# Optimization experiments

Hardware: AMD Instinct MI355X
Metric: run time of the kernel (lower is better)

Reference implementation:

```python
import jax, jax.numpy as jnp
import numpy as np
from jax.scipy.special import logsumexp

B, L, M, D = 8192, 1024, 128, 2  # batch, hilbert.size, bond dim, local_size
MACHINE_POW = 2


def setup_inputs() -> dict:
    key = jax.random.key(0)
    k1, k2 = jax.random.split(key)
    # configurations in the zero-magnetization sector: each row is a permutation
    # of L//2 zeros and L//2 ones (constrained HomogeneousHilbert)
    base = jnp.tile(jnp.arange(D, dtype=jnp.int32), L // D)  # (L,)
    inputs = jax.vmap(lambda k: jax.random.permutation(k, base))(jax.random.split(k1, B))
    # variational parameters epsilon: (local_size, M, size); centered at 1 so the
    # length-L multiplicative cache chain stays in fp32 range
    epsilon = 1.0 + 0.02 * jax.random.normal(k2, (D, M, L), dtype=jnp.float32)
    return {"inputs": inputs, "epsilon": epsilon}


def _conditionals(inputs, epsilon):
    # inputs: (B, L) int in [0, D); epsilon: (D, M, L)
    Bn, Ln = inputs.shape
    Dn, Mn, _ = epsilon.shape
    half = Ln // 2

    def scan_fun(carry, index):
        cache, n_spins = carry                       # (B, D, M), (B, D)
        prev = inputs[:, (index - 1) % Ln]           # (B,) previous-site state
        params_i = epsilon[:, :, index]              # (D, M)
        # irregular gather: cache[b, prev[b], :]
        gathered = jnp.take_along_axis(cache, prev[:, None, None], axis=1)[:, 0, :]  # (B, M)
        prods = params_i[None, :, :] * gathered[:, None, :]  # (B, D, M)
        log_psi = jnp.sum(prods, axis=-1)            # (B, D) sum over bond dim
        n_spins = jnp.where(index > 0,
                            n_spins + jax.nn.one_hot(prev, Dn, dtype=jnp.int32),
                            n_spins)
        # zero-magnetization renormalization: -inf once a local state is exhausted
        renorm = jnp.log(jnp.heaviside((half - n_spins).astype(log_psi.dtype), 0.0))
        return (prods, n_spins), log_psi + renorm

    cache0 = jnp.ones((Bn, Dn, Mn), epsilon.dtype)
    n0 = jnp.zeros((Bn, Dn), jnp.int32)
    _, log_psi = jax.lax.scan(scan_fun, (cache0, n0), jnp.arange(Ln))
    return jnp.transpose(log_psi, (1, 0, 2))  # (B, L, D)


def reference(inputs, epsilon):
    lp = _conditionals(inputs, epsilon)  # (B, L, D)
    # normalize conditionals over local states (machine_pow = 2)
    lp = lp - (1.0 / MACHINE_POW) * logsumexp(MACHINE_POW * lp, axis=-1, keepdims=True)
    # pick the log-conditional of the actual configuration at each site
    sel = jnp.take_along_axis(lp, inputs[:, :, None], axis=2)[:, :, 0]  # (B, L)
    # n_symm = 1 (default apply_symmetries): symmetrized logsumexp is identity
    return jnp.sum(sel, axis=1)  # (B,) log_psi
```

## Files before the change

### kernel.cpp

```cpp
#include <hip/hip_runtime.h>

typedef unsigned long long u64;
typedef unsigned int uint32;
typedef short short8 __attribute__((ext_vector_type(8)));
typedef float f32x4 __attribute__((ext_vector_type(4)));

#define B_N 8192
#define L_N 1024
#define M_N 128
#define C_N 16
#define CH_N 64
#define HALF_N 512
#define SL 20
#define ROWF (8 * SL)

#define OFF_W    0
#define OFF_R    0x80000
#define OFF_BITS 0x100000
#define OFF_LR   0x208000
#define OFF_RQ   0x248000
#define OFF_T    0x2248000

#define PACK_BLK (B_N * L_N / 256)
#define EPS_BLK  32
#define ZERO_BLK 32

__device__ __forceinline__ unsigned short f32_bf16(float f) {
    union { float f; unsigned u; } x; x.f = f;
    unsigned u = x.u + 0x7FFFu + ((x.u >> 16) & 1u);
    return (unsigned short)(u >> 16);
}
__device__ __forceinline__ float bf16lo(uint32 w) {
    union { unsigned u; float f; } x; x.u = w << 16; return x.f;
}
__device__ __forceinline__ float bf16hi(uint32 w) {
    union { unsigned u; float f; } x; x.u = w & 0xFFFF0000u; return x.f;
}

__global__ __launch_bounds__(256) void k_prep(const int* __restrict__ inp,
        const float* __restrict__ eps, u64* __restrict__ bits,
        float* __restrict__ w, float* __restrict__ r,
        unsigned short* __restrict__ lrT, float* __restrict__ out) {
    int bid = blockIdx.x;
    if (bid < PACK_BLK) {
        int g = bid * 256 + threadIdx.x;
        int v = inp[g];
        u64 m = __ballot(v != 0);
        if ((threadIdx.x & 63) == 0) bits[g >> 6] = m;
        return;
    }
    bid -= PACK_BLK;
    if (bid < EPS_BLK) {
        int wid = threadIdx.x >> 6, lane = threadIdx.x & 63;
        int m = bid * 4 + wid;
        const float* e0 = eps + (size_t)m * L_N + lane * 16;
        const float* e1 = eps + (size_t)(M_N + m) * L_N + lane * 16;
        float a[16], b[16];
        #pragma unroll
        for (int j = 0; j < 16; j += 4) {
            *(float4*)&a[j] = *(const float4*)&e0[j];
            *(float4*)&b[j] = *(const float4*)&e1[j];
        }
        float local = 1.f;
        #pragma unroll
        for (int j = 0; j < 16; ++j) local *= a[j];
        float sc = local;
        #pragma unroll
        for (int d = 1; d < 64; d <<= 1) {
            float up = __shfl_up(sc, d);
            if (lane >= d) sc *= up;
        }
        float prev = __shfl_up(sc, 1);
        float E = (lane == 0) ? 1.f : prev;
        int i0 = lane * 16;
        #pragma unroll
        for (int j = 0; j < 16; ++j) {
            float rat = b[j] / a[j];
            w[(size_t)(i0 + j) * M_N + m] = E * (a[j] - b[j]);
            r[(size_t)(i0 + j) * M_N + m] = rat;
            lrT[(size_t)m * L_N + i0 + j] = f32_bf16(__log2f(rat));
            E *= a[j];
        }
        return;
    }
    bid -= EPS_BLK;
    if (bid < ZERO_BLK) {
        out[bid * 256 + threadIdx.x] = 0.f;
    }
}

__global__ __launch_bounds__(256) void k_slog2(const u64* __restrict__ bits,
        const unsigned short* __restrict__ lrT, unsigned short* __restrict__ Rq,
        int* __restrict__ T) {
    if (blockIdx.x >= 1024) {
        int b = (blockIdx.x - 1024) * 256 + threadIdx.x;
        const u64* brow = bits + (size_t)b * 16;
        int n1 = 0, n0 = 0, Tv = 1024;
        for (int wd = 0; wd < 16; ++wd) {
            u64 x = brow[wd];
            int pc = __popcll(x);
            if (n1 + pc < HALF_N && n0 + (64 - pc) < HALF_N) {
                n1 += pc; n0 += 64 - pc;
                continue;
            }
            int found = 0;
            for (int k = 0; k < 64; ++k) {
                if (n1 >= HALF_N || n0 >= HALF_N) { Tv = wd * 64 + k; found = 1; break; }
                int sb = (int)((x >> k) & 1);
                n1 += sb; n0 += 1 - sb;
            }
            if (!found) Tv = (wd + 1) * 64;
            break;
        }
        T[b] = Tv;
        return;
    }
    int btile = blockIdx.x >> 1;
    int half = blockIdx.x & 1;
    int wid = threadIdx.x >> 6, lane = threadIdx.x & 63;
    int col = lane & 15, quad = lane >> 4;
    int m = (half * 4 + wid) * 16 + col;
    int b_row = btile * 16 + col;
    const u64* brow = bits + (size_t)b_row * 16;
    const unsigned short* lrow = lrT + (size_t)m * L_N;

    f32x4 cum = (f32x4){0.f, 0.f, 0.f, 0.f};

    for (int c = 0; c < C_N; ++c) {
        #pragma unroll
        for (int reg = 0; reg < 4; ++reg) {
            int b = btile * 16 + quad * 4 + reg;
            Rq[((size_t)c * B_N + b) * M_N + m] = f32_bf16(exp2f(cum[reg]));
        }
        u64 wv = brow[c];
        short8 a0, a1;
        #pragma unroll
        for (int j = 0; j < 8; ++j) {
            a0[j] = (short)((((wv >> (quad * 8 + j)) & 1) != 0) ? 0x3F80 : 0);
            a1[j] = (short)((((wv >> (32 + quad * 8 + j)) & 1) != 0) ? 0x3F80 : 0);
        }
        const unsigned short* bp = lrow + c * 64 + quad * 8;
        union { uint4 u; short8 s; } bf0, bf1;
        bf0.u = *(const uint4*)bp;
        bf1.u = *(const uint4*)(bp + 32);
        cum = __builtin_amdgcn_mfma_f32_16x16x32_bf16(a0, bf0.s, cum, 0, 0, 0);
        cum = __builtin_amdgcn_mfma_f32_16x16x32_bf16(a1, bf1.s, cum, 0, 0, 0);
    }
}

__global__ __launch_bounds__(256) void k_main(const u64* __restrict__ bits,
        const float* __restrict__ w, const float* __restrict__ r,
        const unsigned short* __restrict__ Rq, const int* __restrict__ T,
        float* __restrict__ out) {
    __shared__ float wbuf[32 * ROWF];
    __shared__ float rbuf[32 * ROWF];
    int c = blockIdx.x & (C_N - 1);
    int bblk = blockIdx.x >> 4;
    int lane = threadIdx.x & 63, wid = threadIdx.x >> 6;
    int s = lane & 7, g = lane >> 3;
    int b0 = bblk * 128 + wid * 32 + g * 4;
    int b_own = b0 + (s & 3);

    float R[4][16];
    #pragma unroll
    for (int nb = 0; nb < 4; ++nb) {
        const uint4* src = (const uint4*)(Rq + ((size_t)c * B_N + (b0 + nb)) * M_N + s * 16);
        #pragma unroll
        for (int u_ = 0; u_ < 2; ++u_) {
            uint4 pv = src[u_];
            R[nb][u_ * 8 + 0] = bf16lo(pv.x); R[nb][u_ * 8 + 1] = bf16hi(pv.x);
            R[nb][u_ * 8 + 2] = bf16lo(pv.y); R[nb][u_ * 8 + 3] = bf16hi(pv.y);
            R[nb][u_ * 8 + 4] = bf16lo(pv.z); R[nb][u_ * 8 + 5] = bf16hi(pv.z);
            R[nb][u_ * 8 + 6] = bf16lo(pv.w); R[nb][u_ * 8 + 7] = bf16hi(pv.w);
        }
    }
    int Tb = T[b_own];

    float sum = 0.f;
    for (int h = 0; h < 2; ++h) {
        __syncthreads();
        const float4* srcw = (const float4*)(w + ((size_t)c * CH_N + h * 32) * M_N);
        const float4* srcr = (const float4*)(r + ((size_t)c * CH_N + h * 32) * M_N);
        for (int t = threadIdx.x; t < 32 * 32; t += 256) {
            int i = t >> 5, mqd = t & 31;
            int dst = i * ROWF + (mqd >> 2) * SL + (mqd & 3) * 4;
            *(float4*)&wbuf[dst] = srcw[t];
            *(float4*)&rbuf[dst] = srcr[t];
        }
        __syncthreads();

        uint32 wh[4];
        #pragma unroll
        for (int nb = 0; nb < 4; ++nb)
            wh[nb] = (uint32)(bits[(size_t)(b0 + nb) * 16 + c] >> (h * 32));
        uint32 owa = (s & 1) ? wh[1] : wh[0];
        uint32 owb = (s & 1) ? wh[3] : wh[2];
        uint32 ow = (s & 2) ? owb : owa;

        int rel = Tb - (c * CH_N + h * 32);
        uint32 vmask = (rel <= 0) ? 0u : ((rel >= 32) ? 0xFFFFFFFFu : ((1u << rel) - 1u));

        for (int tt = 0; tt < 32; ++tt) {
            int base = tt * ROWF + s * SL;
            f32x4 wa = *(const f32x4*)&wbuf[base];
            f32x4 wb = *(const f32x4*)&wbuf[base + 4];
            f32x4 wc = *(const f32x4*)&wbuf[base + 8];
            f32x4 wd = *(const f32x4*)&wbuf[base + 12];
            float d[4];
            #pragma unroll
            for (int nb = 0; nb < 4; ++nb) {
                d[nb] = R[nb][0] * wa[0] + R[nb][1] * wa[1] + R[nb][2] * wa[2] + R[nb][3] * wa[3]
                      + R[nb][4] * wb[0] + R[nb][5] * wb[1] + R[nb][6] * wb[2] + R[nb][7] * wb[3]
                      + R[nb][8] * wc[0] + R[nb][9] * wc[1] + R[nb][10] * wc[2] + R[nb][11] * wc[3]
                      + R[nb][12] * wd[0] + R[nb][13] * wd[1] + R[nb][14] * wd[2] + R[nb][15] * wd[3];
            }
            float xa = (s & 1) ? d[1] : d[0];
            float ya = (s & 1) ? d[0] : d[1];
            xa += __shfl_xor(ya, 1);
            float xb = (s & 1) ? d[3] : d[2];
            float yb = (s & 1) ? d[2] : d[3];
            xb += __shfl_xor(yb, 1);
            float u2 = (s & 2) ? xb : xa;
            float v2 = (s & 2) ? xa : xb;
            u2 += __shfl_xor(v2, 2);
            u2 += __shfl_xor(u2, 4);
            float Dv = u2;

            int sbit = (ow >> tt) & 1;
            float y = sbit ? Dv : -Dv;
            float contr = -0.5f * __logf(1.f + __expf(2.f * y));
            sum += ((vmask >> tt) & 1) ? contr : 0.f;

            f32x4 ra = *(const f32x4*)&rbuf[base];
            f32x4 rb = *(const f32x4*)&rbuf[base + 4];
            f32x4 rc = *(const f32x4*)&rbuf[base + 8];
            f32x4 rd = *(const f32x4*)&rbuf[base + 12];
            #pragma unroll
            for (int nb = 0; nb < 4; ++nb) {
                if ((wh[nb] >> tt) & 1) {
                    R[nb][0] *= ra[0];  R[nb][1] *= ra[1];  R[nb][2] *= ra[2];  R[nb][3] *= ra[3];
                    R[nb][4] *= rb[0];  R[nb][5] *= rb[1];  R[nb][6] *= rb[2];  R[nb][7] *= rb[3];
                    R[nb][8] *= rc[0];  R[nb][9] *= rc[1];  R[nb][10] *= rc[2]; R[nb][11] *= rc[3];
                    R[nb][12] *= rd[0]; R[nb][13] *= rd[1]; R[nb][14] *= rd[2]; R[nb][15] *= rd[3];
                }
            }
        }
    }
    if (s < 4) atomicAdd(&out[b_own], sum);
}

extern "C" void kernel_launch(void* const* d_in, const int* in_sizes, int n_in,
                              void* d_out, int out_size, void* d_ws, size_t ws_size,
                              hipStream_t stream) {
    const int*   inputs  = (const int*)d_in[0];
    const float* epsilon = (const float*)d_in[1];
    float* out = (float*)d_out;

    char* ws = (char*)d_ws;
    float* w_tab  = (float*)(ws + OFF_W);
    float* r_tab  = (float*)(ws + OFF_R);
    u64*   bits   = (u64*)  (ws + OFF_BITS);
    unsigned short* lrT = (unsigned short*)(ws + OFF_LR);
    unsigned short* Rq  = (unsigned short*)(ws + OFF_RQ);
    int*   T      = (int*)  (ws + OFF_T);

    k_prep<<<PACK_BLK + EPS_BLK + ZERO_BLK, 256, 0, stream>>>(
        inputs, epsilon, bits, w_tab, r_tab, lrT, out);
    k_slog2<<<1024 + 32, 256, 0, stream>>>(bits, lrT, Rq, T);
    k_main<<<(B_N / 128) * C_N, 256, 0, stream>>>(bits, w_tab, r_tab, Rq, T, out);
}
```

Baseline: 182.9 us.

## Switch k_main state and tables to fp16 with packed dot2 and multiplies

The w/r tables and the per-chunk R cache are now stored as fp16, and k_main's dot products use v_dot2 f32-accumulate with packed half multiplies for the cache update. Both 32-row halves of the table are loaded into shared memory once, so the second sync and reload go away, and the bit words are read once. This halves register and LDS footprint, allows two blocks per CU via launch bounds, and halves ALU work per element. The cost is fp16 range and precision on a multiplicative chain of up to 64 steps, which risks overflow or underflow and reduced accuracy compared with bf16 storage and fp32 compute.

New measurement: 186.0 us. No clear change (+1.6%).

```diff
diff --git a/kernel.cpp b/kernel.cpp
--- a/kernel.cpp
+++ b/kernel.cpp
@@ -1,9 +1,11 @@
 #include <hip/hip_runtime.h>
+#include <hip/hip_fp16.h>
 
 typedef unsigned long long u64;
 typedef unsigned int uint32;
 typedef short short8 __attribute__((ext_vector_type(8)));
 typedef float f32x4 __attribute__((ext_vector_type(4)));
+typedef _Float16 h2 __attribute__((ext_vector_type(2)));
 
 #define B_N 8192
 #define L_N 1024
@@ -11,15 +13,13 @@
 #define C_N 16
 #define CH_N 64
 #define HALF_N 512
-#define SL 20
-#define ROWF (8 * SL)
-
-#define OFF_W    0
-#define OFF_R    0x80000
-#define OFF_BITS 0x100000
-#define OFF_LR   0x208000
-#define OFF_RQ   0x248000
-#define OFF_T    0x2248000
+
+#define OFF_W16  0
+#define OFF_R16  0x40000
+#define OFF_BITS 0x80000
+#define OFF_LR   0x180000
+#define OFF_RQ   0x1C0000
+#define OFF_T    0x21C0000
 
 #define PACK_BLK (B_N * L_N / 256)
 #define EPS_BLK  32
@@ -30,16 +30,18 @@
     unsigned u = x.u + 0x7FFFu + ((x.u >> 16) & 1u);
     return (unsigned short)(u >> 16);
 }
-__device__ __forceinline__ float bf16lo(uint32 w) {
-    union { unsigned u; float f; } x; x.u = w << 16; return x.f;
-}
-__device__ __forceinline__ float bf16hi(uint32 w) {
-    union { unsigned u; float f; } x; x.u = w & 0xFFFF0000u; return x.f;
+
+__device__ __forceinline__ float fdot2(h2 a, h2 b, float c) {
+#if __has_builtin(__builtin_amdgcn_fdot2)
+    return __builtin_amdgcn_fdot2(a, b, c, false);
+#else
+    return (float)a[0] * (float)b[0] + (float)a[1] * (float)b[1] + c;
+#endif
 }
 
 __global__ __launch_bounds__(256) void k_prep(const int* __restrict__ inp,
         const float* __restrict__ eps, u64* __restrict__ bits,
-        float* __restrict__ w, float* __restrict__ r,
+        _Float16* __restrict__ w16, _Float16* __restrict__ r16,
         unsigned short* __restrict__ lrT, float* __restrict__ out) {
     int bid = blockIdx.x;
     if (bid < PACK_BLK) {
@@ -76,8 +78,8 @@
         #pragma unroll
         for (int j = 0; j < 16; ++j) {
             float rat = b[j] / a[j];
-            w[(size_t)(i0 + j) * M_N + m] = E * (a[j] - b[j]);
-            r[(size_t)(i0 + j) * M_N + m] = rat;
+            w16[(size_t)(i0 + j) * M_N + m] = (_Float16)(E * (a[j] - b[j]));
+            r16[(size_t)(i0 + j) * M_N + m] = (_Float16)rat;
             lrT[(size_t)m * L_N + i0 + j] = f32_bf16(__log2f(rat));
             E *= a[j];
         }
@@ -90,7 +92,7 @@
 }
 
 __global__ __launch_bounds__(256) void k_slog2(const u64* __restrict__ bits,
-        const unsigned short* __restrict__ lrT, unsigned short* __restrict__ Rq,
+        const unsigned short* __restrict__ lrT, _Float16* __restrict__ Rq,
         int* __restrict__ T) {
     if (blockIdx.x >= 1024) {
         int b = (blockIdx.x - 1024) * 256 + threadIdx.x;
@@ -130,7 +132,7 @@
         #pragma unroll
         for (int reg = 0; reg < 4; ++reg) {
             int b = btile * 16 + quad * 4 + reg;
-            Rq[((size_t)c * B_N + b) * M_N + m] = f32_bf16(exp2f(cum[reg]));
+            Rq[((size_t)c * B_N + b) * M_N + m] = (_Float16)exp2f(cum[reg]);
         }
         u64 wv = brow[c];
         short8 a0, a1;
@@ -148,12 +150,12 @@
     }
 }
 
-__global__ __launch_bounds__(256) void k_main(const u64* __restrict__ bits,
-        const float* __restrict__ w, const float* __restrict__ r,
-        const unsigned short* __restrict__ Rq, const int* __restrict__ T,
+__global__ __launch_bounds__(256, 2) void k_main(const u64* __restrict__ bits,
+        const _Float16* __restrict__ w16, const _Float16* __restrict__ r16,
+        const _Float16* __restrict__ Rq, const int* __restrict__ T,
         float* __restrict__ out) {
-    __shared__ float wbuf[32 * ROWF];
-    __shared__ float rbuf[32 * ROWF];
+    __shared__ _Float16 wbuf[CH_N * M_N];
+    __shared__ _Float16 rbuf[CH_N * M_N];
     int c = blockIdx.x & (C_N - 1);
     int bblk = blockIdx.x >> 4;
     int lane = threadIdx.x & 63, wid = threadIdx.x >> 6;
@@ -161,38 +163,40 @@
     int b0 = bblk * 128 + wid * 32 + g * 4;
     int b_own = b0 + (s & 3);
 
-    float R[4][16];
+    {
+        const uint4* sw = (const uint4*)(w16 + (size_t)c * CH_N * M_N);
+        const uint4* sr = (const uint4*)(r16 + (size_t)c * CH_N * M_N);
+        uint4* dw = (uint4*)wbuf; uint4* dr = (uint4*)rbuf;
+        #pragma unroll
+        for (int t = 0; t < 4; ++t) {
+            dw[threadIdx.x + t * 256] = sw[threadIdx.x + t * 256];
+            dr[threadIdx.x + t * 256] = sr[threadIdx.x + t * 256];
+        }
+    }
+
+    h2 R2[4][8];
     #pragma unroll
     for (int nb = 0; nb < 4; ++nb) {
+        union { uint4 q[2]; h2 h[8]; } P;
         const uint4* src = (const uint4*)(Rq + ((size_t)c * B_N + (b0 + nb)) * M_N + s * 16);
-        #pragma unroll
-        for (int u_ = 0; u_ < 2; ++u_) {
-            uint4 pv = src[u_];
-            R[nb][u_ * 8 + 0] = bf16lo(pv.x); R[nb][u_ * 8 + 1] = bf16hi(pv.x);
-            R[nb][u_ * 8 + 2] = bf16lo(pv.y); R[nb][u_ * 8 + 3] = bf16hi(pv.y);
-            R[nb][u_ * 8 + 4] = bf16lo(pv.z); R[nb][u_ * 8 + 5] = bf16hi(pv.z);
-            R[nb][u_ * 8 + 6] = bf16lo(pv.w); R[nb][u_ * 8 + 7] = bf16hi(pv.w);
-        }
+        P.q[0] = src[0]; P.q[1] = src[1];
+        #pragma unroll
+        for (int j = 0; j < 8; ++j) R2[nb][j] = P.h[j];
     }
     int Tb = T[b_own];
-
+    u64 wb[4];
+    #pragma unroll
+    for (int nb = 0; nb < 4; ++nb) wb[nb] = bits[(size_t)(b0 + nb) * 16 + c];
+
+    __syncthreads();
+
+    const h2 one2 = (h2){(_Float16)1.f, (_Float16)1.f};
     float sum = 0.f;
+    #pragma unroll
     for (int h = 0; h < 2; ++h) {
-        __syncthreads();
-        const float4* srcw = (const float4*)(w + ((size_t)c * CH_N + h * 32) * M_N);
-        const float4* srcr = (const float4*)(r + ((size_t)c * CH_N + h * 32) * M_N);
-        for (int t = threadIdx.x; t < 32 * 32; t += 256) {
-            int i = t >> 5, mqd = t & 31;
-            int dst = i * ROWF + (mqd >> 2) * SL + (mqd & 3) * 4;
-            *(float4*)&wbuf[dst] = srcw[t];
-            *(float4*)&rbuf[dst] = srcr[t];
-        }
-        __syncthreads();
-
         uint32 wh[4];
         #pragma unroll
-        for (int nb = 0; nb < 4; ++nb)
-            wh[nb] = (uint32)(bits[(size_t)(b0 + nb) * 16 + c] >> (h * 32));
+        for (int nb = 0; nb < 4; ++nb) wh[nb] = (uint32)(wb[nb] >> (h * 32));
         uint32 owa = (s & 1) ? wh[1] : wh[0];
         uint32 owb = (s & 1) ? wh[3] : wh[2];
         uint32 ow = (s & 2) ? owb : owa;
@@ -201,18 +205,20 @@
         uint32 vmask = (rel <= 0) ? 0u : ((rel >= 32) ? 0xFFFFFFFFu : ((1u << rel) - 1u));
 
         for (int tt = 0; tt < 32; ++tt) {
-            int base = tt * ROWF + s * SL;
-            f32x4 wa = *(const f32x4*)&wbuf[base];
-            f32x4 wb = *(const f32x4*)&wbuf[base + 4];
-            f32x4 wc = *(const f32x4*)&wbuf[base + 8];
-            f32x4 wd = *(const f32x4*)&wbuf[base + 12];
+            int base = (h * 32 + tt) * M_N + s * 16;
+            union { uint4 q[2]; h2 h[8]; } W, Rr;
+            W.q[0] = *(const uint4*)&wbuf[base];
+            W.q[1] = *((const uint4*)&wbuf[base] + 1);
+            Rr.q[0] = *(const uint4*)&rbuf[base];
+            Rr.q[1] = *((const uint4*)&rbuf[base] + 1);
+
             float d[4];
             #pragma unroll
             for (int nb = 0; nb < 4; ++nb) {
-                d[nb] = R[nb][0] * wa[0] + R[nb][1] * wa[1] + R[nb][2] * wa[2] + R[nb][3] * wa[3]
-                      + R[nb][4] * wb[0] + R[nb][5] * wb[1] + R[nb][6] * wb[2] + R[nb][7] * wb[3]
-                      + R[nb][8] * wc[0] + R[nb][9] * wc[1] + R[nb][10] * wc[2] + R[nb][11] * wc[3]
-                      + R[nb][12] * wd[0] + R[nb][13] * wd[1] + R[nb][14] * wd[2] + R[nb][15] * wd[3];
+                float acc = 0.f;
+                #pragma unroll
+                for (int j = 0; j < 8; ++j) acc = fdot2(R2[nb][j], W.h[j], acc);
+                d[nb] = acc;
             }
             float xa = (s & 1) ? d[1] : d[0];
             float ya = (s & 1) ? d[0] : d[1];
@@ -231,17 +237,13 @@
             float contr = -0.5f * __logf(1.f + __expf(2.f * y));
             sum += ((vmask >> tt) & 1) ? contr : 0.f;
 
-            f32x4 ra = *(const f32x4*)&rbuf[base];
-            f32x4 rb = *(const f32x4*)&rbuf[base + 4];
-            f32x4 rc = *(const f32x4*)&rbuf[base + 8];
-            f32x4 rd = *(const f32x4*)&rbuf[base + 12];
             #pragma unroll
             for (int nb = 0; nb < 4; ++nb) {
-                if ((wh[nb] >> tt) & 1) {
-                    R[nb][0] *= ra[0];  R[nb][1] *= ra[1];  R[nb][2] *= ra[2];  R[nb][3] *= ra[3];
-                    R[nb][4] *= rb[0];  R[nb][5] *= rb[1];  R[nb][6] *= rb[2];  R[nb][7] *= rb[3];
-                    R[nb][8] *= rc[0];  R[nb][9] *= rc[1];  R[nb][10] *= rc[2]; R[nb][11] *= rc[3];
-                    R[nb][12] *= rd[0]; R[nb][13] *= rd[1]; R[nb][14] *= rd[2]; R[nb][15] *= rd[3];
+                bool bit = (wh[nb] >> tt) & 1;
+                #pragma unroll
+                for (int j = 0; j < 8; ++j) {
+                    h2 sel = bit ? Rr.h[j] : one2;
+                    R2[nb][j] *= sel;
                 }
             }
         }
@@ -257,15 +259,15 @@
     float* out = (float*)d_out;
 
     char* ws = (char*)d_ws;
-    float* w_tab  = (float*)(ws + OFF_W);
-    float* r_tab  = (float*)(ws + OFF_R);
+    _Float16* w16 = (_Float16*)(ws + OFF_W16);
+    _Float16* r16 = (_Float16*)(ws + OFF_R16);
     u64*   bits   = (u64*)  (ws + OFF_BITS);
     unsigned short* lrT = (unsigned short*)(ws + OFF_LR);
-    unsigned short* Rq  = (unsigned short*)(ws + OFF_RQ);
+    _Float16* Rq  = (_Float16*)(ws + OFF_RQ);
     int*   T      = (int*)  (ws + OFF_T);
 
     k_prep<<<PACK_BLK + EPS_BLK + ZERO_BLK, 256, 0, stream>>>(
-        inputs, epsilon, bits, w_tab, r_tab, lrT, out);
+        inputs, epsilon, bits, w16, r16, lrT, out);
     k_slog2<<<1024 + 32, 256, 0, stream>>>(bits, lrT, Rq, T);
-    k_main<<<(B_N / 128) * C_N, 256, 0, stream>>>(bits, w_tab, r_tab, Rq, T, out);
-}
+    k_main<<<(B_N / 128) * C_N, 256, 0, stream>>>(bits, w16, r16, Rq, T, out);
+}
```
